# Kernel tuning notes

Measured on AMD Instinct MI355X. Metric: run time of the kernel, lower is better.

## Reference

```python
import jax, jax.numpy as jnp
import numpy as np

EMBED_DIM = 1024
N_HEADS = 16
HEAD_DIM = EMBED_DIM // N_HEADS


def setup_inputs() -> dict:
    key = jax.random.key(0)
    k_x, k_qw, k_qb, k_ow, k_ob = jax.random.split(key, 5)
    s = 1.0 / np.sqrt(EMBED_DIM)
    return {
        "x": jax.random.normal(k_x, (2, 2048, EMBED_DIM), dtype=jnp.float32),
        "qkv_w": jax.random.uniform(k_qw, (3 * EMBED_DIM, EMBED_DIM), jnp.float32, -s, s),
        "qkv_b": jax.random.uniform(k_qb, (3 * EMBED_DIM,), jnp.float32, -s, s),
        "out_w": jax.random.uniform(k_ow, (EMBED_DIM, EMBED_DIM), jnp.float32, -s, s),
        "out_b": jax.random.uniform(k_ob, (EMBED_DIM,), jnp.float32, -s, s),
    }


def reference(x, qkv_w, qkv_b, out_w, out_b):
    B, S, E = x.shape
    # fused QKV projection (torch Linear: x @ W^T + b)
    qkv = x @ qkv_w.T + qkv_b                      # [B,S,3E]
    qkv = qkv.reshape(B, S, N_HEADS, 3 * HEAD_DIM).transpose(0, 2, 1, 3)  # [B,H,S,3d]
    q, k, v = jnp.split(qkv, 3, axis=-1)           # each [B,H,S,d]
    scores = jnp.einsum("bhqd,bhkd->bhqk", q, k) / jnp.sqrt(jnp.float32(HEAD_DIM))
    weights = jax.nn.softmax(scores, axis=-1)      # [B,H,S,S]
    attn = jnp.einsum("bhqk,bhkd->bhqd", weights, v)
    attn = attn.transpose(0, 2, 1, 3).reshape(B, S, E)
    return attn @ out_w.T + out_b
```

## Files before the change

### kernel.cpp

```cpp
#include <hip/hip_runtime.h>
#include <hip/hip_bf16.h>


#define E_DIM   1024
#define NHEADS  16
#define HDIM    64
#define SEQ     2048
#define TOK     4096
#define QKV_DIM 3072
#define QK_STRIDE 2048
#define QSCALE_F 0.18033688011112042f

typedef __attribute__((ext_vector_type(8))) short bf16x8;
typedef __attribute__((ext_vector_type(4))) float f32x4;
typedef __attribute__((ext_vector_type(4))) int   i32x4;
typedef __attribute__((ext_vector_type(2))) int   i32x2;
typedef __attribute__((ext_vector_type(2))) __bf16 bf16x2_t;

#if __has_builtin(__builtin_amdgcn_exp2f)
#define EXP2F(x) __builtin_amdgcn_exp2f(x)
#else
#define EXP2F(x) exp2f(x)
#endif

__device__ __forceinline__ unsigned pack2bf(float a, float b) {
#if __has_builtin(__builtin_amdgcn_cvt_pk_bf16_f32)
    union { bf16x2_t v; unsigned u; } u;
    u.v = __builtin_amdgcn_cvt_pk_bf16_f32(a, b);
    return u.u;
#else
    union { float f; unsigned u; } ua, ub; ua.f = a; ub.f = b;
    unsigned ra = ua.u + 0x7FFF + ((ua.u >> 16) & 1);
    unsigned rb = ub.u + 0x7FFF + ((ub.u >> 16) & 1);
    return (ra >> 16) | (rb & 0xFFFF0000u);
#endif
}

__device__ __forceinline__ unsigned short f2bf(float x) {
    return (unsigned short)(pack2bf(x, x) & 0xFFFFu);
}

__device__ __forceinline__ void load_lds16(const void* g, void* l) {
    __builtin_amdgcn_global_load_lds(
        (const __attribute__((address_space(1))) void*)g,
        (__attribute__((address_space(3))) void*)l, 16, 0, 0);
}

__device__ __forceinline__ bf16x8 lds_read8(const unsigned short* p) {
    union { i32x4 i; bf16x8 b; } u;
    u.i = *(const i32x4*)p;
    return u.b;
}

__device__ __forceinline__ f32x4 mfma16(bf16x8 a, bf16x8 b, f32x4 c) {
    return __builtin_amdgcn_mfma_f32_16x16x32_bf16(a, b, c, 0, 0, 0);
}

__global__ void cast3_kernel(const float* __restrict__ a, unsigned short* __restrict__ oa, int na4,
                             const float* __restrict__ b, unsigned short* __restrict__ ob, int nb4,
                             const float* __restrict__ c, unsigned short* __restrict__ oc) {
    int i = blockIdx.x * blockDim.x + threadIdx.x;
    const float* src; unsigned short* dst; int j;
    if (i < na4)            { src = a; dst = oa; j = i; }
    else if (i < na4 + nb4) { src = b; dst = ob; j = i - na4; }
    else                    { src = c; dst = oc; j = i - na4 - nb4; }
    f32x4 v = ((const f32x4*)src)[j];
    union { i32x2 i2; unsigned u[2]; } o;
    o.u[0] = pack2bf(v.x, v.y);
    o.u[1] = pack2bf(v.z, v.w);
    ((i32x2*)dst)[j] = o.i2;
}

__global__ __launch_bounds__(256, 3)
void gemm_qkv_kernel(const unsigned short* __restrict__ A,
                     const unsigned short* __restrict__ B,
                     const float* __restrict__ bias,
                     unsigned short* __restrict__ qk,
                     unsigned short* __restrict__ vT,
                     int K) {
    __shared__ __align__(16) unsigned short As[128 * 64];
    __shared__ __align__(16) unsigned short Bs[128 * 64];

    const int tid  = threadIdx.x;
    const int wave = tid >> 6, lane = tid & 63;
    const int quad = lane >> 4, l16 = lane & 15;
    const int row0 = blockIdx.y * 128, col0 = blockIdx.x * 128;
    const int wr = (wave >> 1) * 64, wc = (wave & 1) * 64;

    f32x4 acc[4][4];
#pragma unroll
    for (int i = 0; i < 4; ++i)
#pragma unroll
        for (int j = 0; j < 4; ++j) acc[i][j] = (f32x4){0.f, 0.f, 0.f, 0.f};

    const int nkt = K >> 6;
    for (int kt = 0; kt < nkt; ++kt) {
        const int k0 = kt << 6;
#pragma unroll
        for (int i = 0; i < 4; ++i) {
            int p = i * 256 + tid;
            int r = p >> 3;
            int kc = (p & 7) ^ (r & 7);
            load_lds16(A + (size_t)(row0 + r) * K + k0 + kc * 8, &As[p * 8]);
        }
#pragma unroll
        for (int i = 0; i < 4; ++i) {
            int p = i * 256 + tid;
            int r = p >> 3;
            int kc = (p & 7) ^ (r & 7);
            load_lds16(B + (size_t)(col0 + r) * K + k0 + kc * 8, &Bs[p * 8]);
        }
        __syncthreads();

#pragma unroll
        for (int ks = 0; ks < 2; ++ks) {
            bf16x8 af[4], bfr[4];
#pragma unroll
            for (int rb = 0; rb < 4; ++rb) {
                int r_l  = wr + rb * 16 + l16;
                int phys = (ks * 4 + quad) ^ (l16 & 7);
                af[rb] = lds_read8(&As[r_l * 64 + phys * 8]);
            }
#pragma unroll
            for (int cb = 0; cb < 4; ++cb) {
                int r_l  = wc + cb * 16 + l16;
                int phys = (ks * 4 + quad) ^ (l16 & 7);
                bfr[cb] = lds_read8(&Bs[r_l * 64 + phys * 8]);
            }
#pragma unroll
            for (int rb = 0; rb < 4; ++rb)
#pragma unroll
                for (int cb = 0; cb < 4; ++cb)
                    acc[rb][cb] = mfma16(af[rb], bfr[cb], acc[rb][cb]);
        }
        __syncthreads();
    }

#pragma unroll
    for (int rb = 0; rb < 4; ++rb)
#pragma unroll
        for (int cb = 0; cb < 4; ++cb) {
            int col = col0 + wc + cb * 16 + l16;
            int h    = col / 192;
            int part = col - h * 192;
            float bv = bias[col];
            int row_b = row0 + wr + rb * 16 + quad * 4;
            float v[4];
#pragma unroll
            for (int reg = 0; reg < 4; ++reg) v[reg] = acc[rb][cb][reg] + bv;
            if (part < 128) {
                float sc = (part < 64) ? QSCALE_F : 1.0f;
                size_t base = (size_t)h * 128 + part;
#pragma unroll
                for (int reg = 0; reg < 4; ++reg)
                    qk[(size_t)(row_b + reg) * QK_STRIDE + base] = f2bf(v[reg] * sc);
            } else {
                int i  = part - 128;
                int b  = row_b >> 11;
                int s  = row_b & 2047;
                i32x2 pk;
                pk.x = (int)pack2bf(v[0], v[1]);
                pk.y = (int)pack2bf(v[2], v[3]);
                *(i32x2*)&vT[(((size_t)(b * 16 + h)) * 64 + i) * SEQ + s] = pk;
            }
        }
}

__global__ __launch_bounds__(256, 2)
void gemm2_kernel(const unsigned short* __restrict__ A,
                  const unsigned short* __restrict__ B,
                  const float* __restrict__ bias,
                  float* __restrict__ C, int M, int N, int K) {
    __shared__ __align__(16) unsigned short As[128 * 64];
    __shared__ __align__(16) unsigned short Bs[64 * 64];

    const int tid  = threadIdx.x;
    const int wave = tid >> 6, lane = tid & 63;
    const int quad = lane >> 4, l16 = lane & 15;
    const int row0 = blockIdx.y * 128, col0 = blockIdx.x * 64;
    const int wr = wave * 32;

    f32x4 acc[2][4];
#pragma unroll
    for (int i = 0; i < 2; ++i)
#pragma unroll
        for (int j = 0; j < 4; ++j) acc[i][j] = (f32x4){0.f, 0.f, 0.f, 0.f};

    const int nkt = K >> 6;
    for (int kt = 0; kt < nkt; ++kt) {
        const int k0 = kt << 6;
#pragma unroll
        for (int i = 0; i < 4; ++i) {
            int p = i * 256 + tid;
            int r = p >> 3;
            int kc = (p & 7) ^ (r & 7);
            load_lds16(A + (size_t)(row0 + r) * K + k0 + kc * 8, &As[p * 8]);
        }
#pragma unroll
        for (int i = 0; i < 2; ++i) {
            int p = i * 256 + tid;
            int r = p >> 3;
            int kc = (p & 7) ^ (r & 7);
            load_lds16(B + (size_t)(col0 + r) * K + k0 + kc * 8, &Bs[p * 8]);
        }
        __syncthreads();

#pragma unroll
        for (int ks = 0; ks < 2; ++ks) {
            bf16x8 af[2], bfr[4];
#pragma unroll
            for (int rb = 0; rb < 2; ++rb) {
                int r_l  = wr + rb * 16 + l16;
                int phys = (ks * 4 + quad) ^ (l16 & 7);
                af[rb] = lds_read8(&As[r_l * 64 + phys * 8]);
            }
#pragma unroll
            for (int cb = 0; cb < 4; ++cb) {
                int r_l  = cb * 16 + l16;
                int phys = (ks * 4 + quad) ^ (l16 & 7);
                bfr[cb] = lds_read8(&Bs[r_l * 64 + phys * 8]);
            }
#pragma unroll
            for (int rb = 0; rb < 2; ++rb)
#pragma unroll
                for (int cb = 0; cb < 4; ++cb)
                    acc[rb][cb] = mfma16(af[rb], bfr[cb], acc[rb][cb]);
        }
        __syncthreads();
    }

#pragma unroll
    for (int rb = 0; rb < 2; ++rb)
#pragma unroll
        for (int cb = 0; cb < 4; ++cb) {
            int col = col0 + cb * 16 + l16;
            float bv = bias[col];
#pragma unroll
            for (int reg = 0; reg < 4; ++reg) {
                int row = row0 + wr + rb * 16 + quad * 4 + reg;
                C[(size_t)row * N + col] = acc[rb][cb][reg] + bv;
            }
        }
}


#define STAGE(BUF, KT) do {                                                    \
    const unsigned short* kbase_ =                                             \
        qk + (rowbase + (KT) * 128) * QK_STRIDE + h * 128 + 64;                \
    const unsigned short* vbase_ = vT + (size_t)bh * 64 * SEQ + (KT) * 128;    \
    _Pragma("unroll") for (int i_ = 0; i_ < 2; ++i_) {                         \
        int p_ = i_ * 512 + tid; int r_ = p_ >> 3;                             \
        int kc_ = (p_ & 7) ^ (r_ & 7);                                         \
        load_lds16(kbase_ + r_ * QK_STRIDE + kc_ * 8, &Ks[BUF][p_ * 8]);       \
    }                                                                          \
    _Pragma("unroll") for (int i_ = 0; i_ < 2; ++i_) {                         \
        int p_ = i_ * 512 + tid; int r_ = p_ >> 4;                             \
        int c_ = (p_ & 15) ^ (r_ & 15);                                        \
        load_lds16(vbase_ + r_ * SEQ + c_ * 8, &Vs[BUF][p_ * 8]);              \
    }                                                                          \
} while (0)

#define COMPUTE_TILE(BUF) do {                                                 \
    constexpr int KO_ = (BUF) * 8192;         \
    f32x4 s[8];                                                                \
    _Pragma("unroll") for (int cb = 0; cb < 8; ++cb)                           \
        s[cb] = (f32x4){0.f, 0.f, 0.f, 0.f};                                   \
    __builtin_amdgcn_s_setprio(1);                                             \
    _Pragma("unroll") for (int cb = 0; cb < 8; ++cb) {                         \
        bf16x8 kf0 = lds_read8(Kb0 + KO_ + cb * 1024);                         \
        s[cb] = mfma16(kf0, qf[0], s[cb]);                                     \
    }                                                                          \
    _Pragma("unroll") for (int cb = 0; cb < 8; ++cb) {                         \
        bf16x8 kf1 = lds_read8(Kb1 + KO_ + cb * 1024);                         \
        s[cb] = mfma16(kf1, qf[1], s[cb]);                                     \
    }                                                                          \
    __builtin_amdgcn_s_setprio(0);                                             \
    float rs = 0.f;                                                            \
    _Pragma("unroll") for (int cb = 0; cb < 8; ++cb)                           \
        _Pragma("unroll") for (int r = 0; r < 4; ++r) {                        \
            float pv = EXP2F(s[cb][r]);                                        \
            s[cb][r] = pv;                                                     \
            rs += pv;                                                          \
        }                                                                      \
    rs += __shfl_xor(rs, 16);                                                  \
    rs += __shfl_xor(rs, 32);                                                  \
    l_s += rs;                                                                 \
    _Pragma("unroll") for (int half = 0; half < 2; ++half) {                   \
        _Pragma("unroll") for (int c4 = 0; c4 < 4; ++c4) {                     \
            int cb = half * 4 + c4;                                            \
            i32x2 pk;                                                          \
            pk.x = (int)pack2bf(s[cb][0], s[cb][1]);                           \
            pk.y = (int)pack2bf(s[cb][2], s[cb][3]);                           \
            *(i32x2*)Pw[c4] = pk;                                              \
        }                                                                      \
        __asm__ volatile("s_waitcnt lgkmcnt(0)" ::: "memory");                 \
        __builtin_amdgcn_s_setprio(1);                                         \
        {                                                                      \
            bf16x8 pf0 = lds_read8(Pr0);                                       \
            _Pragma("unroll") for (int ib = 0; ib < 4; ++ib) {                 \
                bf16x8 vf = lds_read8(Vb[half * 2 + 0] + KO_ + ib * 2048);     \
                o[ib] = mfma16(pf0, vf, o[ib]);                                \
            }                                                                  \
            bf16x8 pf1 = lds_read8(Pr1);                                       \
            _Pragma("unroll") for (int ib = 0; ib < 4; ++ib) {                 \
                bf16x8 vf = lds_read8(Vb[half * 2 + 1] + KO_ + ib * 2048);     \
                o[ib] = mfma16(pf1, vf, o[ib]);                                \
            }                                                                  \
        }                                                                      \
        __builtin_amdgcn_s_setprio(0);                                         \
    }                                                                          \
} while (0)

__global__ __launch_bounds__(512, 4)
void attn_kernel(const unsigned short* __restrict__ qk,
                 const unsigned short* __restrict__ vT,
                 unsigned short* __restrict__ attn) {
    __shared__ __align__(16) unsigned short Ks[2][128 * 64];
    __shared__ __align__(16) unsigned short Vs[2][64 * 128];
    __shared__ __align__(16) unsigned short Ps[8][16 * 64];

    const int tid  = threadIdx.x;
    const int wave = tid >> 6, lane = tid & 63;
    const int quad = lane >> 4, l16 = lane & 15;
    const int bh = blockIdx.y;
    const int b = bh >> 4, h = bh & 15;
    const int q0 = blockIdx.x * 128;
    const size_t rowbase = (size_t)b * SEQ;
    const int qtok = q0 + wave * 16 + l16;

    const int sw3 = l16 & 7;
    const unsigned short* Kb0 = &Ks[0][l16 * 64 + ((quad ^ sw3) * 8)];
    const unsigned short* Kb1 = &Ks[0][l16 * 64 + (((4 + quad) ^ sw3) * 8)];
    const unsigned short* Vb[4] = {
        &Vs[0][l16 * 128 + (((0 * 4 + quad) ^ l16) * 8)],
        &Vs[0][l16 * 128 + (((1 * 4 + quad) ^ l16) * 8)],
        &Vs[0][l16 * 128 + (((2 * 4 + quad) ^ l16) * 8)],
        &Vs[0][l16 * 128 + (((3 * 4 + quad) ^ l16) * 8)] };
    unsigned short* Pw[4];
#pragma unroll
    for (int c4 = 0; c4 < 4; ++c4)
        Pw[c4] = &Ps[wave][l16 * 64 + (((c4 * 2 + (quad >> 1)) ^ sw3) * 8) + (quad & 1) * 4];
    const unsigned short* Pr0 = &Ps[wave][l16 * 64 + ((quad ^ sw3) * 8)];
    const unsigned short* Pr1 = &Ps[wave][l16 * 64 + (((4 + quad) ^ sw3) * 8)];

    bf16x8 qf[2];
#pragma unroll
    for (int ks = 0; ks < 2; ++ks) {
        const unsigned short* p =
            qk + (rowbase + qtok) * QK_STRIDE + h * 128 + ks * 32 + quad * 8;
        union { i32x4 i; bf16x8 b; } u;
        u.i = *(const i32x4*)p;
        qf[ks] = u.b;
    }

    f32x4 o[4];
#pragma unroll
    for (int ib = 0; ib < 4; ++ib) o[ib] = (f32x4){0.f, 0.f, 0.f, 0.f};
    float l_s = 0.f;

    STAGE(0, 0);
#pragma unroll 1
    for (int kt = 0; kt < SEQ / 128; kt += 2) {
        STAGE(1, kt + 1);
        __asm__ volatile("s_waitcnt vmcnt(4)" ::: "memory");
        __builtin_amdgcn_s_barrier();
        COMPUTE_TILE(0);
        __builtin_amdgcn_s_barrier();
        if (kt + 2 < SEQ / 128) {
            STAGE(0, kt + 2);
            __asm__ volatile("s_waitcnt vmcnt(4)" ::: "memory");
        } else {
            __asm__ volatile("s_waitcnt vmcnt(0)" ::: "memory");
        }
        __builtin_amdgcn_s_barrier();
        COMPUTE_TILE(1);
        __builtin_amdgcn_s_barrier();
    }

    float il[4];
#pragma unroll
    for (int r = 0; r < 4; ++r) il[r] = 1.0f / __shfl(l_s, quad * 4 + r);
#pragma unroll
    for (int ib = 0; ib < 4; ++ib)
#pragma unroll
        for (int r = 0; r < 4; ++r) {
            int t = q0 + wave * 16 + quad * 4 + r;
            attn[(rowbase + t) * E_DIM + h * 64 + ib * 16 + l16] =
                f2bf(o[ib][r] * il[r]);
        }
}

extern "C" void kernel_launch(void* const* d_in, const int* in_sizes, int n_in,
                              void* d_out, int out_size, void* d_ws, size_t ws_size,
                              hipStream_t stream) {
    const float* x     = (const float*)d_in[0];
    const float* qkv_w = (const float*)d_in[1];
    const float* qkv_b = (const float*)d_in[2];
    const float* out_w = (const float*)d_in[3];
    const float* out_b = (const float*)d_in[4];

    char* ws = (char*)d_ws;
    unsigned short* xb   = (unsigned short*)(ws);
    unsigned short* wqkv = (unsigned short*)(ws + 8388608);
    unsigned short* wout = (unsigned short*)(ws + 14680064);
    unsigned short* qk   = (unsigned short*)(ws + 16777216);
    unsigned short* attn = (unsigned short*)(ws + 33554432);
    unsigned short* vT   = (unsigned short*)(ws + 41943040);

    cast3_kernel<<<8192, 256, 0, stream>>>(x, xb, 1048576,
                                           qkv_w, wqkv, 786432,
                                           out_w, wout);

    gemm_qkv_kernel<<<dim3(24, 32), 256, 0, stream>>>(
        xb, wqkv, qkv_b, qk, vT, E_DIM);

    attn_kernel<<<dim3(16, 32), 512, 0, stream>>>(qk, vT, attn);

    gemm2_kernel<<<dim3(16, 32), 256, 0, stream>>>(
        attn, wout, out_b, (float*)d_out, TOK, E_DIM, E_DIM);
}
```

Measured before the change: 183.6 us.

## Software-pipeline QK^T of next tile with softmax-PV of current tile

Restructures the attention loop so the QK^T MFMAs for tile k+1 are issued alongside the exp/PV work for tile k, using two score register sets. K and V loads are split and issued at separate barriers with precomputed pointers. Block indices are also remapped so consecutive blocks go to different (b,h) groups, and launch bounds drop to 2 blocks per SM. The aim is to hide MFMA and memory latency behind the softmax work, at the cost of extra registers and lower occupancy.

```diff
diff --git a/kernel.cpp b/kernel.cpp
--- a/kernel.cpp
+++ b/kernel.cpp
@@ -244,53 +244,40 @@
 }
 
 
-#define STAGE(BUF, KT) do {                                                    \
-    const unsigned short* kbase_ =                                             \
-        qk + (rowbase + (KT) * 128) * QK_STRIDE + h * 128 + 64;                \
-    const unsigned short* vbase_ = vT + (size_t)bh * 64 * SEQ + (KT) * 128;    \
-    _Pragma("unroll") for (int i_ = 0; i_ < 2; ++i_) {                         \
-        int p_ = i_ * 512 + tid; int r_ = p_ >> 3;                             \
-        int kc_ = (p_ & 7) ^ (r_ & 7);                                         \
-        load_lds16(kbase_ + r_ * QK_STRIDE + kc_ * 8, &Ks[BUF][p_ * 8]);       \
-    }                                                                          \
-    _Pragma("unroll") for (int i_ = 0; i_ < 2; ++i_) {                         \
-        int p_ = i_ * 512 + tid; int r_ = p_ >> 4;                             \
-        int c_ = (p_ & 15) ^ (r_ & 15);                                        \
-        load_lds16(vbase_ + r_ * SEQ + c_ * 8, &Vs[BUF][p_ * 8]);              \
-    }                                                                          \
-} while (0)
-
-#define COMPUTE_TILE(BUF) do {                                                 \
-    constexpr int KO_ = (BUF) * 8192;         \
-    f32x4 s[8];                                                                \
+#define QK_TILE(SC, PC) do {                                                   \
     _Pragma("unroll") for (int cb = 0; cb < 8; ++cb)                           \
-        s[cb] = (f32x4){0.f, 0.f, 0.f, 0.f};                                   \
+        SC[cb] = (f32x4){0.f, 0.f, 0.f, 0.f};                                  \
     __builtin_amdgcn_s_setprio(1);                                             \
     _Pragma("unroll") for (int cb = 0; cb < 8; ++cb) {                         \
-        bf16x8 kf0 = lds_read8(Kb0 + KO_ + cb * 1024);                         \
-        s[cb] = mfma16(kf0, qf[0], s[cb]);                                     \
+        bf16x8 kf0 = lds_read8(Kb0 + (PC) * 8192 + cb * 1024);                 \
+        SC[cb] = mfma16(kf0, qf[0], SC[cb]);                                   \
     }                                                                          \
     _Pragma("unroll") for (int cb = 0; cb < 8; ++cb) {                         \
-        bf16x8 kf1 = lds_read8(Kb1 + KO_ + cb * 1024);                         \
-        s[cb] = mfma16(kf1, qf[1], s[cb]);                                     \
+        bf16x8 kf1 = lds_read8(Kb1 + (PC) * 8192 + cb * 1024);                 \
+        SC[cb] = mfma16(kf1, qf[1], SC[cb]);                                   \
     }                                                                          \
     __builtin_amdgcn_s_setprio(0);                                             \
-    float rs = 0.f;                                                            \
+} while (0)
+
+#define SMPV_TILE(SP, VB) do {                                                 \
     _Pragma("unroll") for (int cb = 0; cb < 8; ++cb)                           \
-        _Pragma("unroll") for (int r = 0; r < 4; ++r) {                        \
-            float pv = EXP2F(s[cb][r]);                                        \
-            s[cb][r] = pv;                                                     \
-            rs += pv;                                                          \
-        }                                                                      \
-    rs += __shfl_xor(rs, 16);                                                  \
-    rs += __shfl_xor(rs, 32);                                                  \
-    l_s += rs;                                                                 \
+        _Pragma("unroll") for (int r = 0; r < 4; ++r)                          \
+            SP[cb][r] = EXP2F(SP[cb][r]);                                      \
+    {                                                                          \
+        f32x4 t0 = SP[0] + SP[1], t1 = SP[2] + SP[3];                          \
+        f32x4 t2 = SP[4] + SP[5], t3 = SP[6] + SP[7];                          \
+        t0 += t1; t2 += t3; t0 += t2;                                          \
+        float rs = (t0[0] + t0[1]) + (t0[2] + t0[3]);                          \
+        rs += __shfl_xor(rs, 16);                                              \
+        rs += __shfl_xor(rs, 32);                                              \
+        l_s += rs;                                                             \
+    }                                                                          \
     _Pragma("unroll") for (int half = 0; half < 2; ++half) {                   \
         _Pragma("unroll") for (int c4 = 0; c4 < 4; ++c4) {                     \
             int cb = half * 4 + c4;                                            \
             i32x2 pk;                                                          \
-            pk.x = (int)pack2bf(s[cb][0], s[cb][1]);                           \
-            pk.y = (int)pack2bf(s[cb][2], s[cb][3]);                           \
+            pk.x = (int)pack2bf(SP[cb][0], SP[cb][1]);                         \
+            pk.y = (int)pack2bf(SP[cb][2], SP[cb][3]);                         \
             *(i32x2*)Pw[c4] = pk;                                              \
         }                                                                      \
         __asm__ volatile("s_waitcnt lgkmcnt(0)" ::: "memory");                 \
@@ -298,12 +285,12 @@
         {                                                                      \
             bf16x8 pf0 = lds_read8(Pr0);                                       \
             _Pragma("unroll") for (int ib = 0; ib < 4; ++ib) {                 \
-                bf16x8 vf = lds_read8(Vb[half * 2 + 0] + KO_ + ib * 2048);     \
+                bf16x8 vf = lds_read8(Vb[half * 2 + 0] + (VB) * 8192 + ib * 2048); \
                 o[ib] = mfma16(pf0, vf, o[ib]);                                \
             }                                                                  \
             bf16x8 pf1 = lds_read8(Pr1);                                       \
             _Pragma("unroll") for (int ib = 0; ib < 4; ++ib) {                 \
-                bf16x8 vf = lds_read8(Vb[half * 2 + 1] + KO_ + ib * 2048);     \
+                bf16x8 vf = lds_read8(Vb[half * 2 + 1] + (VB) * 8192 + ib * 2048); \
                 o[ib] = mfma16(pf1, vf, o[ib]);                                \
             }                                                                  \
         }                                                                      \
@@ -311,7 +298,23 @@
     }                                                                          \
 } while (0)
 
-__global__ __launch_bounds__(512, 4)
+#define ATTN_ITER(SC, SP, PC, DO_STAGE) do {                                   \
+    __asm__ volatile("s_waitcnt vmcnt(2)" ::: "memory");                       \
+    __builtin_amdgcn_s_barrier();                                              \
+    if (DO_STAGE) {                                                            \
+        load_lds16(kg[0], lk[0] + ((PC) ^ 1) * 8192); kg[0] += 128 * QK_STRIDE;\
+        load_lds16(kg[1], lk[1] + ((PC) ^ 1) * 8192); kg[1] += 128 * QK_STRIDE;\
+    }                                                                          \
+    QK_TILE(SC, PC);                                                           \
+    SMPV_TILE(SP, (PC) ^ 1);                                                   \
+    __builtin_amdgcn_s_barrier();                                              \
+    if (DO_STAGE) {                                                            \
+        load_lds16(vg[0], lv[0] + ((PC) ^ 1) * 8192); vg[0] += 128;            \
+        load_lds16(vg[1], lv[1] + ((PC) ^ 1) * 8192); vg[1] += 128;            \
+    }                                                                          \
+} while (0)
+
+__global__ __launch_bounds__(512, 2)
 void attn_kernel(const unsigned short* __restrict__ qk,
                  const unsigned short* __restrict__ vT,
                  unsigned short* __restrict__ attn) {
@@ -322,9 +325,12 @@
     const int tid  = threadIdx.x;
     const int wave = tid >> 6, lane = tid & 63;
     const int quad = lane >> 4, l16 = lane & 15;
-    const int bh = blockIdx.y;
+
+    const int flat = blockIdx.y * 16 + blockIdx.x;
+    const int swz  = (flat & 7) * 64 + (flat >> 3);
+    const int bh = swz >> 4;
     const int b = bh >> 4, h = bh & 15;
-    const int q0 = blockIdx.x * 128;
+    const int q0 = (swz & 15) * 128;
     const size_t rowbase = (size_t)b * SEQ;
     const int qtok = q0 + wave * 16 + l16;
 
@@ -343,6 +349,19 @@
     const unsigned short* Pr0 = &Ps[wave][l16 * 64 + ((quad ^ sw3) * 8)];
     const unsigned short* Pr1 = &Ps[wave][l16 * 64 + (((4 + quad) ^ sw3) * 8)];
 
+    const unsigned short* kg[2]; unsigned short* lk[2];
+    const unsigned short* vg[2]; unsigned short* lv[2];
+#pragma unroll
+    for (int i = 0; i < 2; ++i) {
+        int p = i * 512 + tid;
+        { int r = p >> 3; int kc = (p & 7) ^ (r & 7);
+          kg[i] = qk + rowbase * QK_STRIDE + h * 128 + 64 + (size_t)r * QK_STRIDE + kc * 8;
+          lk[i] = &Ks[0][p * 8]; }
+        { int r = p >> 4; int c = (p & 15) ^ (r & 15);
+          vg[i] = vT + (size_t)bh * 64 * SEQ + (size_t)r * SEQ + c * 8;
+          lv[i] = &Vs[0][p * 8]; }
+    }
+
     bf16x8 qf[2];
 #pragma unroll
     for (int ks = 0; ks < 2; ++ks) {
@@ -358,24 +377,30 @@
     for (int ib = 0; ib < 4; ++ib) o[ib] = (f32x4){0.f, 0.f, 0.f, 0.f};
     float l_s = 0.f;
 
-    STAGE(0, 0);
+    f32x4 sA[8], sB[8];
+
+#pragma unroll
+    for (int i = 0; i < 2; ++i) { load_lds16(kg[i], lk[i]); kg[i] += 128 * QK_STRIDE; }
+#pragma unroll
+    for (int i = 0; i < 2; ++i) { load_lds16(vg[i], lv[i]); vg[i] += 128; }
+    __asm__ volatile("s_waitcnt vmcnt(0)" ::: "memory");
+    __builtin_amdgcn_s_barrier();
+    QK_TILE(sA, 0);
+#pragma unroll
+    for (int i = 0; i < 2; ++i) { load_lds16(kg[i], lk[i] + 8192); kg[i] += 128 * QK_STRIDE; }
+#pragma unroll
+    for (int i = 0; i < 2; ++i) { load_lds16(vg[i], lv[i] + 8192); vg[i] += 128; }
+
 #pragma unroll 1
-    for (int kt = 0; kt < SEQ / 128; kt += 2) {
-        STAGE(1, kt + 1);
-        __asm__ volatile("s_waitcnt vmcnt(4)" ::: "memory");
-        __builtin_amdgcn_s_barrier();
-        COMPUTE_TILE(0);
-        __builtin_amdgcn_s_barrier();
-        if (kt + 2 < SEQ / 128) {
-            STAGE(0, kt + 2);
-            __asm__ volatile("s_waitcnt vmcnt(4)" ::: "memory");
-        } else {
-            __asm__ volatile("s_waitcnt vmcnt(0)" ::: "memory");
-        }
-        __builtin_amdgcn_s_barrier();
-        COMPUTE_TILE(1);
-        __builtin_amdgcn_s_barrier();
+    for (int kt = 1; kt < 15; kt += 2) {
+        ATTN_ITER(sB, sA, 1, 1);
+        ATTN_ITER(sA, sB, 0, 1);
     }
+    ATTN_ITER(sB, sA, 1, 0);
+
+    __asm__ volatile("s_waitcnt vmcnt(0)" ::: "memory");
+    __builtin_amdgcn_s_barrier();
+    SMPV_TILE(sB, 1);
 
     float il[4];
 #pragma unroll
```

After: 190.3 us. +3.6%, slower.

## Keep attention probabilities in registers via permuted V layout, add XCD-aware block swizzles

Applied to the files above, without the earlier changes.

The QKV GEMM epilogue now writes V^T with a permuted sequence index, so the attention kernel can feed exponentiated scores straight from MFMA accumulators as the A operand of the PV MFMA. This removes the per-wave P round trip through LDS (write, waitcnt, read) and the Ps shared buffer. The row-sum is also restructured as a vector tree reduction. All three kernels remap block indices so that blocks sharing data land on the same XCD for L2 reuse, and the K/V staging uses precomputed incrementing pointers. The risk lies in getting the permutation exactly right for correctness, and in the extra register pressure.

```diff
diff --git a/kernel.cpp b/kernel.cpp
--- a/kernel.cpp
+++ b/kernel.cpp
@@ -84,7 +84,11 @@
     const int tid  = threadIdx.x;
     const int wave = tid >> 6, lane = tid & 63;
     const int quad = lane >> 4, l16 = lane & 15;
-    const int row0 = blockIdx.y * 128, col0 = blockIdx.x * 128;
+    const int flat = blockIdx.y * 24 + blockIdx.x;
+    const int xcd = flat & 7, idx = flat >> 3;
+    const int row_blk = (xcd >> 1) * 8 + idx / 12;
+    const int col_blk = (xcd & 1) * 12 + idx % 12;
+    const int row0 = row_blk * 128, col0 = col_blk * 128;
     const int wr = (wave >> 1) * 64, wc = (wave & 1) * 64;
 
     f32x4 acc[4][4];
@@ -157,11 +161,14 @@
             } else {
                 int i  = part - 128;
                 int b  = row_b >> 11;
-                int s  = row_b & 2047;
+                int s0 = row_b & 2047;
+                int kk = s0 & 127;
+                int cc = kk >> 4, qq = (kk >> 2) & 3;
+                int sp = (s0 & ~127) | ((cc >> 1) << 5) | (qq << 3) | ((cc & 1) << 2);
                 i32x2 pk;
                 pk.x = (int)pack2bf(v[0], v[1]);
                 pk.y = (int)pack2bf(v[2], v[3]);
-                *(i32x2*)&vT[(((size_t)(b * 16 + h)) * 64 + i) * SEQ + s] = pk;
+                *(i32x2*)&vT[(((size_t)(b * 16 + h)) * 64 + i) * SEQ + sp] = pk;
             }
         }
 }
@@ -177,7 +184,11 @@
     const int tid  = threadIdx.x;
     const int wave = tid >> 6, lane = tid & 63;
     const int quad = lane >> 4, l16 = lane & 15;
-    const int row0 = blockIdx.y * 128, col0 = blockIdx.x * 64;
+    const int flat = blockIdx.y * 16 + blockIdx.x;
+    const int xcd = flat & 7, idx = flat >> 3;
+    const int row_blk = (xcd >> 1) * 8 + (idx >> 3);
+    const int col_blk = (xcd & 1) * 8 + (idx & 7);
+    const int row0 = row_blk * 128, col0 = col_blk * 64;
     const int wr = wave * 32;
 
     f32x4 acc[2][4];
@@ -244,24 +255,15 @@
 }
 
 
-#define STAGE(BUF, KT) do {                                                    \
-    const unsigned short* kbase_ =                                             \
-        qk + (rowbase + (KT) * 128) * QK_STRIDE + h * 128 + 64;                \
-    const unsigned short* vbase_ = vT + (size_t)bh * 64 * SEQ + (KT) * 128;    \
-    _Pragma("unroll") for (int i_ = 0; i_ < 2; ++i_) {                         \
-        int p_ = i_ * 512 + tid; int r_ = p_ >> 3;                             \
-        int kc_ = (p_ & 7) ^ (r_ & 7);                                         \
-        load_lds16(kbase_ + r_ * QK_STRIDE + kc_ * 8, &Ks[BUF][p_ * 8]);       \
-    }                                                                          \
-    _Pragma("unroll") for (int i_ = 0; i_ < 2; ++i_) {                         \
-        int p_ = i_ * 512 + tid; int r_ = p_ >> 4;                             \
-        int c_ = (p_ & 15) ^ (r_ & 15);                                        \
-        load_lds16(vbase_ + r_ * SEQ + c_ * 8, &Vs[BUF][p_ * 8]);              \
-    }                                                                          \
+#define STAGE_KV(BUF) do {                                                     \
+    load_lds16(kg[0], lk[0] + (BUF) * 8192); kg[0] += 128 * QK_STRIDE;         \
+    load_lds16(kg[1], lk[1] + (BUF) * 8192); kg[1] += 128 * QK_STRIDE;         \
+    load_lds16(vg[0], lv[0] + (BUF) * 8192); vg[0] += 128;                     \
+    load_lds16(vg[1], lv[1] + (BUF) * 8192); vg[1] += 128;                     \
 } while (0)
 
 #define COMPUTE_TILE(BUF) do {                                                 \
-    constexpr int KO_ = (BUF) * 8192;         \
+    constexpr int KO_ = (BUF) * 8192;                                          \
     f32x4 s[8];                                                                \
     _Pragma("unroll") for (int cb = 0; cb < 8; ++cb)                           \
         s[cb] = (f32x4){0.f, 0.f, 0.f, 0.f};                                   \
@@ -275,40 +277,32 @@
         s[cb] = mfma16(kf1, qf[1], s[cb]);                                     \
     }                                                                          \
     __builtin_amdgcn_s_setprio(0);                                             \
-    float rs = 0.f;                                                            \
     _Pragma("unroll") for (int cb = 0; cb < 8; ++cb)                           \
-        _Pragma("unroll") for (int r = 0; r < 4; ++r) {                        \
-            float pv = EXP2F(s[cb][r]);                                        \
-            s[cb][r] = pv;                                                     \
-            rs += pv;                                                          \
+        _Pragma("unroll") for (int r = 0; r < 4; ++r)                          \
+            s[cb][r] = EXP2F(s[cb][r]);                                        \
+    {                                                                          \
+        f32x4 t0 = s[0] + s[1], t1 = s[2] + s[3];                              \
+        f32x4 t2 = s[4] + s[5], t3 = s[6] + s[7];                              \
+        t0 += t1; t2 += t3; t0 += t2;                                          \
+        float rs = (t0[0] + t0[1]) + (t0[2] + t0[3]);                          \
+        rs += __shfl_xor(rs, 16);                                              \
+        rs += __shfl_xor(rs, 32);                                              \
+        l_s += rs;                                                             \
+    }                                                                          \
+    __builtin_amdgcn_s_setprio(1);                                             \
+    _Pragma("unroll") for (int ks2 = 0; ks2 < 4; ++ks2) {                      \
+        union { i32x4 i; bf16x8 b; } pu;                                       \
+        pu.i.x = (int)pack2bf(s[2 * ks2][0], s[2 * ks2][1]);                   \
+        pu.i.y = (int)pack2bf(s[2 * ks2][2], s[2 * ks2][3]);                   \
+        pu.i.z = (int)pack2bf(s[2 * ks2 + 1][0], s[2 * ks2 + 1][1]);           \
+        pu.i.w = (int)pack2bf(s[2 * ks2 + 1][2], s[2 * ks2 + 1][3]);           \
+        bf16x8 pf = pu.b;                                                      \
+        _Pragma("unroll") for (int ib = 0; ib < 4; ++ib) {                     \
+            bf16x8 vf = lds_read8(Vb[ks2] + KO_ + ib * 2048);                  \
+            o[ib] = mfma16(pf, vf, o[ib]);                                     \
         }                                                                      \
-    rs += __shfl_xor(rs, 16);                                                  \
-    rs += __shfl_xor(rs, 32);                                                  \
-    l_s += rs;                                                                 \
-    _Pragma("unroll") for (int half = 0; half < 2; ++half) {                   \
-        _Pragma("unroll") for (int c4 = 0; c4 < 4; ++c4) {                     \
-            int cb = half * 4 + c4;                                            \
-            i32x2 pk;                                                          \
-            pk.x = (int)pack2bf(s[cb][0], s[cb][1]);                           \
-            pk.y = (int)pack2bf(s[cb][2], s[cb][3]);                           \
-            *(i32x2*)Pw[c4] = pk;                                              \
-        }                                                                      \
-        __asm__ volatile("s_waitcnt lgkmcnt(0)" ::: "memory");                 \
-        __builtin_amdgcn_s_setprio(1);                                         \
-        {                                                                      \
-            bf16x8 pf0 = lds_read8(Pr0);                                       \
-            _Pragma("unroll") for (int ib = 0; ib < 4; ++ib) {                 \
-                bf16x8 vf = lds_read8(Vb[half * 2 + 0] + KO_ + ib * 2048);     \
-                o[ib] = mfma16(pf0, vf, o[ib]);                                \
-            }                                                                  \
-            bf16x8 pf1 = lds_read8(Pr1);                                       \
-            _Pragma("unroll") for (int ib = 0; ib < 4; ++ib) {                 \
-                bf16x8 vf = lds_read8(Vb[half * 2 + 1] + KO_ + ib * 2048);     \
-                o[ib] = mfma16(pf1, vf, o[ib]);                                \
-            }                                                                  \
-        }                                                                      \
-        __builtin_amdgcn_s_setprio(0);                                         \
     }                                                                          \
+    __builtin_amdgcn_s_setprio(0);                                             \
 } while (0)
 
 __global__ __launch_bounds__(512, 4)
@@ -317,14 +311,16 @@
                  unsigned short* __restrict__ attn) {
     __shared__ __align__(16) unsigned short Ks[2][128 * 64];
     __shared__ __align__(16) unsigned short Vs[2][64 * 128];
-    __shared__ __align__(16) unsigned short Ps[8][16 * 64];
 
     const int tid  = threadIdx.x;
     const int wave = tid >> 6, lane = tid & 63;
     const int quad = lane >> 4, l16 = lane & 15;
-    const int bh = blockIdx.y;
+
+    const int flat = blockIdx.y * 16 + blockIdx.x;
+    const int swz  = (flat & 7) * 64 + (flat >> 3);
+    const int bh = swz >> 4;
     const int b = bh >> 4, h = bh & 15;
-    const int q0 = blockIdx.x * 128;
+    const int q0 = (swz & 15) * 128;
     const size_t rowbase = (size_t)b * SEQ;
     const int qtok = q0 + wave * 16 + l16;
 
@@ -336,12 +332,19 @@
         &Vs[0][l16 * 128 + (((1 * 4 + quad) ^ l16) * 8)],
         &Vs[0][l16 * 128 + (((2 * 4 + quad) ^ l16) * 8)],
         &Vs[0][l16 * 128 + (((3 * 4 + quad) ^ l16) * 8)] };
-    unsigned short* Pw[4];
-#pragma unroll
-    for (int c4 = 0; c4 < 4; ++c4)
-        Pw[c4] = &Ps[wave][l16 * 64 + (((c4 * 2 + (quad >> 1)) ^ sw3) * 8) + (quad & 1) * 4];
-    const unsigned short* Pr0 = &Ps[wave][l16 * 64 + ((quad ^ sw3) * 8)];
-    const unsigned short* Pr1 = &Ps[wave][l16 * 64 + (((4 + quad) ^ sw3) * 8)];
+
+    const unsigned short* kg[2]; unsigned short* lk[2];
+    const unsigned short* vg[2]; unsigned short* lv[2];
+#pragma unroll
+    for (int i = 0; i < 2; ++i) {
+        int p = i * 512 + tid;
+        { int r = p >> 3; int kc = (p & 7) ^ (r & 7);
+          kg[i] = qk + (rowbase) * QK_STRIDE + h * 128 + 64 + (size_t)r * QK_STRIDE + kc * 8;
+          lk[i] = &Ks[0][p * 8]; }
+        { int r = p >> 4; int c = (p & 15) ^ (r & 15);
+          vg[i] = vT + (size_t)bh * 64 * SEQ + (size_t)r * SEQ + c * 8;
+          lv[i] = &Vs[0][p * 8]; }
+    }
 
     bf16x8 qf[2];
 #pragma unroll
@@ -358,16 +361,16 @@
     for (int ib = 0; ib < 4; ++ib) o[ib] = (f32x4){0.f, 0.f, 0.f, 0.f};
     float l_s = 0.f;
 
-    STAGE(0, 0);
+    STAGE_KV(0);
 #pragma unroll 1
     for (int kt = 0; kt < SEQ / 128; kt += 2) {
-        STAGE(1, kt + 1);
+        STAGE_KV(1);
         __asm__ volatile("s_waitcnt vmcnt(4)" ::: "memory");
         __builtin_amdgcn_s_barrier();
         COMPUTE_TILE(0);
         __builtin_amdgcn_s_barrier();
         if (kt + 2 < SEQ / 128) {
-            STAGE(0, kt + 2);
+            STAGE_KV(0);
             __asm__ volatile("s_waitcnt vmcnt(4)" ::: "memory");
         } else {
             __asm__ volatile("s_waitcnt vmcnt(0)" ::: "memory");
```

Result: faster. 175.2 us (-4.6%).
